# Kernel optimization log

Measured on AMD Instinct MI355X. Metric: run time of the kernel, lower is better.

The kernel has to match this reference:

```python
import jax, jax.numpy as jnp
import numpy as np

HIDDEN = 2048
NUM_HEADS = 16
NUM_KV_HEADS = 4
HEAD_DIM = HIDDEN // NUM_HEADS  # 128
WINDOW = 512
THETA = 10000.0
BATCH = 4
SEQ = 2048
NEG = -1e30


def _apply_rope(x, pos, theta):
    # x: [T, H, D] with interleaved even/odd rotation, matching the torch strided slicing
    half = x.shape[-1] // 2
    inv_freq = 1.0 / (theta ** (jnp.arange(half, dtype=jnp.float32) / half))
    ang = pos.astype(jnp.float32)[:, None] * inv_freq[None, :]          # [T, half]
    cos = jnp.cos(ang)[:, None, :]                                       # [T, 1, half]
    sin = jnp.sin(ang)[:, None, :]
    xe = x[..., 0::2].astype(jnp.float32)
    xo = x[..., 1::2].astype(jnp.float32)
    re = xe * cos - xo * sin
    ro = xe * sin + xo * cos
    out = jnp.stack([re, ro], axis=-1).reshape(x.shape)                  # re-interleave
    return out.astype(x.dtype)


def setup_inputs() -> dict:
    key = jax.random.key(0)
    ks = jax.random.split(key, 5)
    sc = 1.0 / np.sqrt(HIDDEN)
    hidden_states = jax.random.normal(ks[0], (BATCH * SEQ, HIDDEN), dtype=jnp.float32)
    q_w = jax.random.normal(ks[1], (HIDDEN, NUM_HEADS * HEAD_DIM), dtype=jnp.float32) * sc
    k_w = jax.random.normal(ks[2], (HIDDEN, NUM_KV_HEADS * HEAD_DIM), dtype=jnp.float32) * sc
    v_w = jax.random.normal(ks[3], (HIDDEN, NUM_KV_HEADS * HEAD_DIM), dtype=jnp.float32) * sc
    o_w = jax.random.normal(ks[4], (HIDDEN, HIDDEN), dtype=jnp.float32) * sc
    position_ids = jnp.tile(jnp.arange(SEQ, dtype=jnp.int32), BATCH)     # restart per sequence
    cu_seqlens = jnp.arange(BATCH + 1, dtype=jnp.int32) * SEQ
    return {
        "hidden_states": hidden_states, "q_w": q_w, "k_w": k_w, "v_w": v_w, "o_w": o_w,
        "position_ids": position_ids, "cu_seqlens": cu_seqlens, "max_seq_len": SEQ,
    }


def reference(hidden_states, q_w, k_w, v_w, o_w, position_ids, cu_seqlens, max_seq_len):
    T = hidden_states.shape[0]
    B = cu_seqlens.shape[0] - 1
    S = T // B  # equal-length packing
    groups = NUM_HEADS // NUM_KV_HEADS

    q = (hidden_states @ q_w).reshape(T, NUM_HEADS, HEAD_DIM)
    k = (hidden_states @ k_w).reshape(T, NUM_KV_HEADS, HEAD_DIM)
    v = (hidden_states @ v_w).reshape(T, NUM_KV_HEADS, HEAD_DIM)

    q = _apply_rope(q, position_ids, THETA)
    k = _apply_rope(k, position_ids, THETA)

    q = q.reshape(B, S, NUM_HEADS, HEAD_DIM)
    k = k.reshape(B, S, NUM_KV_HEADS, HEAD_DIM)
    v = v.reshape(B, S, NUM_KV_HEADS, HEAD_DIM)
    # GQA: expand kv heads to query heads
    k = jnp.repeat(k, groups, axis=2)   # [B, S, H, D]
    v = jnp.repeat(v, groups, axis=2)

    scale = 1.0 / np.sqrt(HEAD_DIM)
    scores = jnp.einsum('bqhd,bkhd->bhqk', q, k) * scale  # [B, H, S, S]

    pos = position_ids.reshape(B, S)
    pq = pos[:, None, :, None]
    pk = pos[:, None, None, :]
    # causal + sliding window (flash window_size=(WINDOW, 0) semantics): q-k in [0, WINDOW]
    allowed = (pk <= pq) & ((pq - pk) <= WINDOW)
    scores = jnp.where(allowed, scores, NEG)

    probs = jax.nn.softmax(scores, axis=-1)
    attn = jnp.einsum('bhqk,bkhd->bqhd', probs, v)        # [B, S, H, D]
    attn = attn.reshape(T, HIDDEN)
    return attn @ o_w
```

## Files before the change

### kernel.cpp

```cpp
#include <hip/hip_runtime.h>
#include <hip/hip_bf16.h>
#include <cstdint>
#include <cstddef>

typedef __bf16 bf16;
typedef __bf16 bf16x2 __attribute__((ext_vector_type(2)));
typedef __bf16 bf16x8 __attribute__((ext_vector_type(8)));
typedef float  f32x4  __attribute__((ext_vector_type(4)));

#define HIDDEN 2048
#define NHEADS 16
#define NKV    4
#define HD     128
#define WINDOW 512

__device__ __forceinline__ void gld16(const void* g, void* s) {
  __builtin_amdgcn_global_load_lds((const __attribute__((address_space(1))) void*)g,
                                   (__attribute__((address_space(3))) void*)s, 16, 0, 0);
}

__device__ __forceinline__ f32x4 mfma16(bf16x8 a, bf16x8 b, f32x4 c) {
  return __builtin_amdgcn_mfma_f32_16x16x32_bf16(a, b, c, 0, 0, 0);
}

__device__ __forceinline__ void barrier_raw() {
  asm volatile("" ::: "memory");
  __builtin_amdgcn_s_barrier();
  asm volatile("" ::: "memory");
}

__global__ __launch_bounds__(256) void cast_f32_bf16(const float* __restrict__ in,
                                                     bf16* __restrict__ out, int n4) {
  int i = blockIdx.x * 256 + threadIdx.x;
  if (i >= n4) return;
  f32x4 v = *(const f32x4*)(in + (size_t)i * 4);
  bf16x2 a, b;
  a[0] = (bf16)v[0]; a[1] = (bf16)v[1];
  b[0] = (bf16)v[2]; b[1] = (bf16)v[3];
  *(bf16x2*)(out + (size_t)i * 4)     = a;
  *(bf16x2*)(out + (size_t)i * 4 + 2) = b;
}

__global__ __launch_bounds__(256) void transpose_cast(const float* __restrict__ in,
                                                      bf16* __restrict__ out, int R, int C) {
  __shared__ float tile[32][33];
  int c0 = blockIdx.x * 32, r0 = blockIdx.y * 32;
  int tx = threadIdx.x, ty = threadIdx.y;
  #pragma unroll
  for (int i = 0; i < 4; ++i)
    tile[ty + i * 8][tx] = in[(size_t)(r0 + ty + i * 8) * C + c0 + tx];
  __syncthreads();
  #pragma unroll
  for (int i = 0; i < 4; ++i)
    out[(size_t)(c0 + ty + i * 8) * R + r0 + tx] = (bf16)tile[tx][ty + i * 8];
}

__device__ __forceinline__ void stage128x32(const bf16* __restrict__ A,
                                            const bf16* __restrict__ Bt,
                                            bf16* sA, bf16* sB,
                                            int m0, int n0, int K, int kt, int tid) {
  int wbase = tid & ~63;
  #pragma unroll
  for (int r = 0; r < 2; ++r) {
    int e = (r * 256 + tid) * 8;
    int row = e >> 5, col = e & 31;
    gld16(A  + (size_t)(m0 + row) * K + (size_t)kt * 32 + col,
          sA + (size_t)(r * 256 + wbase) * 8);
    gld16(Bt + (size_t)(n0 + row) * K + (size_t)kt * 32 + col,
          sB + (size_t)(r * 256 + wbase) * 8);
  }
}

__global__ __launch_bounds__(256) void gemm_bt(const bf16* __restrict__ A,
                                               const bf16* __restrict__ Bt,
                                               void* __restrict__ Cv,
                                               bf16* __restrict__ Vtout,
                                               int M, int N, int K, int outMode) {
  __shared__ bf16 sA[2][128 * 32];
  __shared__ bf16 sB[2][128 * 32];
  int nb = N >> 7;
  int perx = (int)gridDim.x >> 3;
  int bid0 = (int)blockIdx.x;
  int swzb = (bid0 & 7) * perx + (bid0 >> 3);
  int bm = swzb / nb, bn = swzb % nb;
  int m0 = bm << 7, n0 = bn << 7;
  int tid = threadIdx.x;
  int lane = tid & 63, w = tid >> 6;
  int li = lane & 15, g = lane >> 4, g8 = g * 8;
  int wm = w >> 1, wn = w & 1;
  f32x4 acc[4][4] = {};
  int NT = K >> 5;

  stage128x32(A, Bt, sA[0], sB[0], m0, n0, K, 0, tid);
  for (int kt = 0; kt < NT; ++kt) {
    int cur = kt & 1;
    asm volatile("s_waitcnt vmcnt(0)" ::: "memory");
    barrier_raw();
    if (kt + 1 < NT)
      stage128x32(A, Bt, sA[cur ^ 1], sB[cur ^ 1], m0, n0, K, kt + 1, tid);
    bf16x8 af[4], bv[4];
    #pragma unroll
    for (int mt = 0; mt < 4; ++mt)
      af[mt] = *(const bf16x8*)&sA[cur][(wm * 64 + mt * 16 + li) * 32 + g8];
    #pragma unroll
    for (int nt = 0; nt < 4; ++nt)
      bv[nt] = *(const bf16x8*)&sB[cur][(wn * 64 + nt * 16 + li) * 32 + g8];
    #pragma unroll
    for (int mt = 0; mt < 4; ++mt)
      #pragma unroll
      for (int nt = 0; nt < 4; ++nt)
        acc[mt][nt] = mfma16(af[mt], bv[nt], acc[mt][nt]);
  }
  #pragma unroll
  for (int mt = 0; mt < 4; ++mt)
    #pragma unroll
    for (int nt = 0; nt < 4; ++nt)
      #pragma unroll
      for (int j = 0; j < 4; ++j) {
        int row = m0 + wm * 64 + mt * 16 + g * 4 + j;
        int col = n0 + wn * 64 + nt * 16 + li;
        float v = acc[mt][nt][j];
        if (outMode == 0)      ((bf16*)Cv)[(size_t)row * N + col] = (bf16)v;
        else if (outMode == 1) ((bf16*)Cv)[(size_t)col * M + row] = (bf16)v;
        else if (outMode == 2) ((float*)Cv)[(size_t)row * N + col] = v;
        else {
          if (col < 512) ((bf16*)Cv)[(size_t)row * 512 + col] = (bf16)v;
          else           Vtout[(size_t)(col - 512) * M + row] = (bf16)v;
        }
      }
}

template<int RSP>
__device__ __forceinline__ void stage_quad(const bf16* __restrict__ G,
                                           bf16* __restrict__ sbuf,
                                           int grow0, int K, int k0, int half, int tid) {
  int w = tid >> 6, lane = tid & 63;
  int rl = lane >> 3;
  int col = ((lane & 7) ^ rl) * 8;
  #pragma unroll
  for (int r = 0; r < 2; ++r) {
    int lr0 = r * 64 + w * 8;
    int row0 = (lr0 & (RSP - 1)) + half * RSP + (lr0 / RSP) * 2 * RSP;
    gld16(G + (size_t)(grow0 + row0 + rl) * K + k0 + col,
          sbuf + row0 * 64);
  }
}

__global__ __launch_bounds__(512, 2) void gemm256(const bf16* __restrict__ A,
                                                  const bf16* __restrict__ Bt,
                                                  void* __restrict__ Cv,
                                                  int M, int N, int K, int outMode) {
  __shared__ bf16 sA[2][256 * 64];
  __shared__ bf16 sB[2][256 * 64];
  int nb = N >> 8;
  int cpx = (int)gridDim.x >> 3;
  int bid = (int)blockIdx.x;
  int swzb = (bid & 7) * cpx + (bid >> 3);
  int bm = swzb / nb, bn = swzb % nb;
  int m0 = bm << 8, n0 = bn << 8;
  int tid = threadIdx.x, lane = tid & 63, w = tid >> 6;
  int li = lane & 15, g = lane >> 4;
  int wm = w >> 2, wn = w & 3;
  int swz = (li & 7);

  f32x4 acc[8][4] = {};
  bf16x8 af[4][2];
  bf16x8 bv[2][2][2];

  int NT = K >> 6;

  stage_quad<64>(A,  sA[0], m0, K, 0, 0, tid);
  stage_quad<32>(Bt, sB[0], n0, K, 0, 0, tid);
  stage_quad<32>(Bt, sB[0], n0, K, 0, 1, tid);
  stage_quad<64>(A,  sA[0], m0, K, 0, 1, tid);

#define VMW(n) asm volatile("s_waitcnt vmcnt(" #n ")" ::: "memory")
#define SBAR() __builtin_amdgcn_sched_barrier(0)
#define LGKM(n) { asm volatile("s_waitcnt lgkmcnt(" #n ")" ::: "memory"); \
  __builtin_amdgcn_sched_barrier(0); }
#define LOAD_A256(mh) { _Pragma("unroll") for (int mf = 0; mf < 4; ++mf) \
  _Pragma("unroll") for (int ks = 0; ks < 2; ++ks) { \
    int row = wm * 128 + (mh) * 64 + mf * 16 + li; \
    af[mf][ks] = *(const bf16x8*)&sA[cur][row * 64 + ((ks * 4 + g) ^ swz) * 8]; } }
#define LOAD_B256(nh) { _Pragma("unroll") for (int nf = 0; nf < 2; ++nf) \
  _Pragma("unroll") for (int ks = 0; ks < 2; ++ks) { \
    int row = wn * 64 + (nh) * 32 + nf * 16 + li; \
    bv[nh][nf][ks] = *(const bf16x8*)&sB[cur][row * 64 + ((ks * 4 + g) ^ swz) * 8]; } }
#define MFMA_PH(mh, nh) { \
  __builtin_amdgcn_s_setprio(1); \
  _Pragma("unroll") for (int mf = 0; mf < 4; ++mf) \
  _Pragma("unroll") for (int nf = 0; nf < 2; ++nf) \
  _Pragma("unroll") for (int ks = 0; ks < 2; ++ks) \
    acc[(mh) * 4 + mf][(nh) * 2 + nf] = \
      mfma16(af[mf][ks], bv[nh][nf][ks], acc[(mh) * 4 + mf][(nh) * 2 + nf]); \
  __builtin_amdgcn_s_setprio(0); }

  int cur = 0;
  for (int t = 0; t < NT; ++t) {
    int nxt = cur ^ 1;
    bool pre = (t + 1 < NT);
    int k1 = (t + 1) << 6;
    VMW(0);
    barrier_raw();
    if (pre) stage_quad<64>(A, sA[nxt], m0, K, k1, 0, tid);
    LOAD_A256(0); LOAD_B256(0);
    SBAR();
    LOAD_B256(1);
    if (pre) stage_quad<32>(Bt, sB[nxt], n0, K, k1, 0, tid);
    LGKM(4);
    MFMA_PH(0, 0);
    if (pre) stage_quad<32>(Bt, sB[nxt], n0, K, k1, 1, tid);
    LGKM(0);
    MFMA_PH(0, 1);
    LOAD_A256(1);
    if (pre) stage_quad<64>(A, sA[nxt], m0, K, k1, 1, tid);
    LGKM(0);
    MFMA_PH(1, 1);
    MFMA_PH(1, 0);
    cur = nxt;
  }
#undef VMW
#undef SBAR
#undef LGKM
#undef LOAD_A256
#undef LOAD_B256
#undef MFMA_PH

  #pragma unroll
  for (int mi = 0; mi < 8; ++mi)
    #pragma unroll
    for (int ni = 0; ni < 4; ++ni)
      #pragma unroll
      for (int j = 0; j < 4; ++j) {
        int row = m0 + wm * 128 + mi * 16 + g * 4 + j;
        int col = n0 + wn * 64 + ni * 16 + li;
        float v = acc[mi][ni][j];
        if (outMode == 2) ((float*)Cv)[(size_t)row * N + col] = v;
        else              ((bf16*)Cv)[(size_t)row * N + col] = (bf16)v;
      }
}

__global__ __launch_bounds__(256) void rope_both(bf16* __restrict__ Qb,
                                                 bf16* __restrict__ Kb,
                                                 const int* __restrict__ pos, int T) {
  int idx = blockIdx.x * 256 + threadIdx.x;
  int total_q = T * NHEADS * 64;
  int total   = total_q + T * NKV * 64;
  if (idx >= total) return;
  bf16* X; int heads, local;
  if (idx < total_q) { X = Qb; heads = NHEADS; local = idx; }
  else               { X = Kb; heads = NKV;    local = idx - total_q; }
  int i = local & 63;
  int rest = local >> 6;
  int hh = rest % heads;
  int t = rest / heads;
  float inv = expf((float)i * (-9.210340371976184f / 64.0f));
  float ang = (float)pos[t] * inv;
  float s, c;
  sincosf(ang, &s, &c);
  bf16* p = X + ((size_t)t * heads + hh) * HD + 2 * i;
  bf16x2 xv = *(const bf16x2*)p;
  float xe = (float)xv[0], xo = (float)xv[1];
  bf16x2 r;
  r[0] = (bf16)(xe * c - xo * s);
  r[1] = (bf16)(xe * s + xo * c);
  *(bf16x2*)p = r;
}

__global__ __launch_bounds__(512) void attn_kernel(const bf16* __restrict__ Q,
                                                   const bf16* __restrict__ Kb,
                                                   const bf16* __restrict__ Vt,
                                                   const int* __restrict__ pos,
                                                   const int* __restrict__ cu,
                                                   bf16* __restrict__ O, int T, int B) {
  __shared__ bf16 sK[2][64 * 128];
  __shared__ bf16 sV[2][128 * 64];
  __shared__ bf16 sP[8][16 * 40];
  int bid = blockIdx.x;
  int nqb = T >> 6;
  int kvh = bid / nqb;
  int u   = bid % nqb;
  int qb  = (u & 7) * (nqb >> 3) + (u >> 3);
  int q0 = qb * 64;
  int tid = threadIdx.x, lane = tid & 63, w = tid >> 6;
  int hh = w & 3, rh = w >> 2;
  int h = kvh * 4 + hh;
  int li = lane & 15, g = lane >> 4, g8 = g * 8;
  int rb0 = q0 + rh * 32;

  int seq_start = 0, seq_end = T;
  for (int b = 0; b < B; ++b) {
    int a = cu[b], e = cu[b + 1];
    if (q0 >= a && q0 < e) { seq_start = a; seq_end = e; }
  }

  bf16x8 qf[2][4];
  #pragma unroll
  for (int grp = 0; grp < 2; ++grp)
    #pragma unroll
    for (int kd = 0; kd < 4; ++kd)
      qf[grp][kd] = *(const bf16x8*)(Q + (size_t)(rb0 + grp * 16 + li) * HIDDEN
                                     + h * HD + kd * 32 + g8);

  int pq[2][4], pmin[2], pmax[2];
  #pragma unroll
  for (int grp = 0; grp < 2; ++grp) {
    #pragma unroll
    for (int j = 0; j < 4; ++j) pq[grp][j] = pos[rb0 + grp * 16 + g * 4 + j];
    pmin[grp] = pos[rb0 + grp * 16];
    pmax[grp] = pos[rb0 + grp * 16 + 15];
  }

  float lsum[2][4] = {};
  f32x4 acc[2][8] = {};
  int kstart = q0 - WINDOW;
  if (kstart < seq_start) kstart = seq_start;
  int kend = q0 + 64;
  if (kend > seq_end) kend = seq_end;
  const float scale = 0.08838834764831845f;
  int nt = (kend - kstart) >> 6;

#define STAGE(kb_, buf_) { \
  _Pragma("unroll") for (int r = 0; r < 2; ++r) { \
    int n = r * 512 + tid; \
    int krow = n >> 4, kc = (n & 15) ^ (krow & 7); \
    gld16(Kb + (size_t)((kb_) + krow) * (NKV * HD) + kvh * HD + kc * 8, \
          &sK[buf_][(size_t)(r * 512 + (tid & ~63)) * 8]); \
    int vd = n >> 3, vc = (n & 7) ^ (vd & 7); \
    gld16(Vt + (size_t)(kvh * HD + vd) * T + (kb_) + vc * 8, \
          &sV[buf_][(size_t)(r * 512 + (tid & ~63)) * 8]); } }
#define VMW(n) asm volatile("s_waitcnt vmcnt(" #n ")" ::: "memory")

  STAGE(kstart, 0);
  for (int t = 0; t < nt; ++t) {
    int kb0 = kstart + t * 64;
    int cur = t & 1;
    VMW(0);
    barrier_raw();
    if (t + 1 < nt) STAGE(kb0 + 64, cur ^ 1);

    #pragma unroll
    for (int hhalf = 0; hhalf < 2; ++hhalf) {
      int kb = kb0 + hhalf * 32;
      int pkf = pos[kb], pkl = pos[kb + 31];
      int pk0 = pos[kb + li], pk1 = pos[kb + 16 + li];
      #pragma unroll
      for (int grp = 0; grp < 2; ++grp) {
        if (pkf > pmax[grp] || pkl < pmin[grp] - WINDOW) continue;
        f32x4 s0v = {0.f, 0.f, 0.f, 0.f}, s1v = {0.f, 0.f, 0.f, 0.f};
        #pragma unroll
        for (int kd = 0; kd < 4; ++kd) {
          int c0 = (kd * 4 + g) ^ (li & 7);
          bf16x8 b0 = *(const bf16x8*)&sK[cur][(hhalf * 32 + li) * 128 + c0 * 8];
          bf16x8 b1 = *(const bf16x8*)&sK[cur][(hhalf * 32 + 16 + li) * 128 + c0 * 8];
          s0v = mfma16(qf[grp][kd], b0, s0v);
          s1v = mfma16(qf[grp][kd], b1, s1v);
        }
        bool interior = (pkl <= pmin[grp]) && (pmax[grp] - pkf <= WINDOW);
        if (interior) {
          #pragma unroll
          for (int j = 0; j < 4; ++j) {
            float p0 = __expf(s0v[j] * scale);
            float p1 = __expf(s1v[j] * scale);
            lsum[grp][j] += p0 + p1;
            sP[w][(g * 4 + j) * 40 + li]      = (bf16)p0;
            sP[w][(g * 4 + j) * 40 + 16 + li] = (bf16)p1;
          }
        } else {
          #pragma unroll
          for (int j = 0; j < 4; ++j) {
            int d0 = pq[grp][j] - pk0, d1 = pq[grp][j] - pk1;
            float p0 = (d0 >= 0 && d0 <= WINDOW) ? __expf(s0v[j] * scale) : 0.f;
            float p1 = (d1 >= 0 && d1 <= WINDOW) ? __expf(s1v[j] * scale) : 0.f;
            lsum[grp][j] += p0 + p1;
            sP[w][(g * 4 + j) * 40 + li]      = (bf16)p0;
            sP[w][(g * 4 + j) * 40 + 16 + li] = (bf16)p1;
          }
        }
        bf16x8 pa = *(const bf16x8*)&sP[w][li * 40 + g8];
        #pragma unroll
        for (int dt = 0; dt < 8; ++dt) {
          int d = dt * 16 + li;
          int vc2 = (hhalf * 4 + g) ^ (d & 7);
          bf16x8 vf = *(const bf16x8*)&sV[cur][d * 64 + vc2 * 8];
          acc[grp][dt] = mfma16(pa, vf, acc[grp][dt]);
        }
      }
    }
  }
#undef STAGE
#undef VMW

  #pragma unroll
  for (int grp = 0; grp < 2; ++grp)
    #pragma unroll
    for (int j = 0; j < 4; ++j) {
      float rs = lsum[grp][j];
      rs += __shfl_xor(rs, 1);
      rs += __shfl_xor(rs, 2);
      rs += __shfl_xor(rs, 4);
      rs += __shfl_xor(rs, 8);
      float invl = 1.0f / rs;
      size_t base = (size_t)(rb0 + grp * 16 + g * 4 + j) * HIDDEN + h * HD;
      #pragma unroll
      for (int dt = 0; dt < 8; ++dt)
        O[base + dt * 16 + li] = (bf16)(acc[grp][dt][j] * invl);
    }
}

extern "C" void kernel_launch(void* const* d_in, const int* in_sizes, int n_in,
                              void* d_out, int out_size, void* d_ws, size_t ws_size,
                              hipStream_t stream) {
  const float* X  = (const float*)d_in[0];
  const float* qw = (const float*)d_in[1];
  const float* kw = (const float*)d_in[2];
  const float* vw = (const float*)d_in[3];
  const float* ow = (const float*)d_in[4];
  const int* pos = (const int*)d_in[5];
  const int* cu  = (const int*)d_in[6];
  int T = in_sizes[0] / HIDDEN;
  int B = in_sizes[6] - 1;
  float* out = (float*)d_out;

  bf16* ws = (bf16*)d_ws;
  size_t off = 0;
  bf16* Xb    = ws + off; off += (size_t)T * HIDDEN;
  bf16* Qb    = ws + off; off += (size_t)T * HIDDEN;
  bf16* Kb    = ws + off; off += (size_t)T * (NKV * HD);
  bf16* Vt    = ws + off; off += (size_t)T * (NKV * HD);
  bf16* qwT   = ws + off; off += (size_t)HIDDEN * HIDDEN;
  bf16* kvwT  = ws + off; off += (size_t)1024 * HIDDEN;
  bf16* owT   = ws + off; off += (size_t)HIDDEN * HIDDEN;

  cast_f32_bf16<<<(T * HIDDEN / 4 + 255) / 256, 256, 0, stream>>>(X, Xb, T * HIDDEN / 4);

  dim3 tb(32, 8);
  transpose_cast<<<dim3(HIDDEN / 32, HIDDEN / 32), tb, 0, stream>>>(qw, qwT, HIDDEN, HIDDEN);
  transpose_cast<<<dim3(512 / 32, HIDDEN / 32), tb, 0, stream>>>(kw, kvwT, HIDDEN, 512);
  transpose_cast<<<dim3(512 / 32, HIDDEN / 32), tb, 0, stream>>>(vw, kvwT + (size_t)512 * HIDDEN, HIDDEN, 512);
  transpose_cast<<<dim3(HIDDEN / 32, HIDDEN / 32), tb, 0, stream>>>(ow, owT, HIDDEN, HIDDEN);

  gemm256<<<(T / 256) * (HIDDEN / 256), 512, 0, stream>>>(Xb, qwT, Qb, T, HIDDEN, HIDDEN, 0);
  gemm_bt<<<(T / 128) * (1024 / 128), 256, 0, stream>>>(Xb, kvwT, Kb, Vt, T, 1024, HIDDEN, 3);

  rope_both<<<(T * (NHEADS + NKV) * 64 + 255) / 256, 256, 0, stream>>>(Qb, Kb, pos, T);

  attn_kernel<<<(T / 64) * NKV, 512, 0, stream>>>(Qb, Kb, Vt, pos, cu, Qb, T, B);

  gemm256<<<(T / 256) * (HIDDEN / 256), 512, 0, stream>>>(Qb, owT, out, T, HIDDEN, HIDDEN, 2);
}
```

Measured before the change: 320.5 us.

## Double GEMM K-tile to 64 with XOR-swizzled LDS layout

Each GEMM k-step now stages a 128x64 tile instead of 128x32, halving the number of barrier/wait iterations. An XOR swizzle of the 16-byte chunk index by row is applied on both the global-to-LDS store and the fragment reads, to avoid LDS bank conflicts that the wider 128-byte row stride would otherwise cause. This doubles LDS use to 64KB per block and raises register pressure from the extra fragments, which may lower occupancy.

```diff
diff --git a/kernel.cpp b/kernel.cpp
--- a/kernel.cpp
+++ b/kernel.cpp
@@ -55,19 +55,20 @@
     out[(size_t)(c0 + ty + i * 8) * R + r0 + tx] = (bf16)tile[tx][ty + i * 8];
 }
 
-__device__ __forceinline__ void stage128x32(const bf16* __restrict__ A,
+__device__ __forceinline__ void stage128x64(const bf16* __restrict__ A,
                                             const bf16* __restrict__ Bt,
                                             bf16* sA, bf16* sB,
                                             int m0, int n0, int K, int kt, int tid) {
-  int wbase = tid & ~63;
-  #pragma unroll
-  for (int r = 0; r < 2; ++r) {
-    int e = (r * 256 + tid) * 8;
-    int row = e >> 5, col = e & 31;
-    gld16(A  + (size_t)(m0 + row) * K + (size_t)kt * 32 + col,
-          sA + (size_t)(r * 256 + wbase) * 8);
-    gld16(Bt + (size_t)(n0 + row) * K + (size_t)kt * 32 + col,
-          sB + (size_t)(r * 256 + wbase) * 8);
+  int wb = (tid & ~63) * 8;
+  #pragma unroll
+  for (int r = 0; r < 4; ++r) {
+    int n = r * 256 + tid;
+    int row = n >> 3;
+    int c = (n & 7) ^ (row & 7);
+    gld16(A  + (size_t)(m0 + row) * K + (size_t)kt * 64 + c * 8,
+          sA + (size_t)(r * 256 * 8) + wb);
+    gld16(Bt + (size_t)(n0 + row) * K + (size_t)kt * 64 + c * 8,
+          sB + (size_t)(r * 256 * 8) + wb);
   }
 }
 
@@ -76,8 +77,8 @@
                                                void* __restrict__ Cv,
                                                bf16* __restrict__ Vtout,
                                                int M, int N, int K, int outMode) {
-  __shared__ bf16 sA[2][128 * 32];
-  __shared__ bf16 sB[2][128 * 32];
+  __shared__ bf16 sA[2][128 * 64];
+  __shared__ bf16 sB[2][128 * 64];
   int nb = N >> 7;
   int perx = (int)gridDim.x >> 3;
   int bid0 = (int)blockIdx.x;
@@ -86,30 +87,39 @@
   int m0 = bm << 7, n0 = bn << 7;
   int tid = threadIdx.x;
   int lane = tid & 63, w = tid >> 6;
-  int li = lane & 15, g = lane >> 4, g8 = g * 8;
+  int li = lane & 15, g = lane >> 4;
   int wm = w >> 1, wn = w & 1;
+  int swz = li & 7;
   f32x4 acc[4][4] = {};
-  int NT = K >> 5;
-
-  stage128x32(A, Bt, sA[0], sB[0], m0, n0, K, 0, tid);
+  int NT = K >> 6;
+
+  stage128x64(A, Bt, sA[0], sB[0], m0, n0, K, 0, tid);
   for (int kt = 0; kt < NT; ++kt) {
     int cur = kt & 1;
     asm volatile("s_waitcnt vmcnt(0)" ::: "memory");
     barrier_raw();
     if (kt + 1 < NT)
-      stage128x32(A, Bt, sA[cur ^ 1], sB[cur ^ 1], m0, n0, K, kt + 1, tid);
-    bf16x8 af[4], bv[4];
+      stage128x64(A, Bt, sA[cur ^ 1], sB[cur ^ 1], m0, n0, K, kt + 1, tid);
+    bf16x8 af[4][2], bv[4][2];
     #pragma unroll
     for (int mt = 0; mt < 4; ++mt)
-      af[mt] = *(const bf16x8*)&sA[cur][(wm * 64 + mt * 16 + li) * 32 + g8];
+      #pragma unroll
+      for (int ks = 0; ks < 2; ++ks)
+        af[mt][ks] = *(const bf16x8*)&sA[cur][(wm * 64 + mt * 16 + li) * 64
+                                              + ((ks * 4 + g) ^ swz) * 8];
     #pragma unroll
     for (int nt = 0; nt < 4; ++nt)
-      bv[nt] = *(const bf16x8*)&sB[cur][(wn * 64 + nt * 16 + li) * 32 + g8];
+      #pragma unroll
+      for (int ks = 0; ks < 2; ++ks)
+        bv[nt][ks] = *(const bf16x8*)&sB[cur][(wn * 64 + nt * 16 + li) * 64
+                                              + ((ks * 4 + g) ^ swz) * 8];
     #pragma unroll
     for (int mt = 0; mt < 4; ++mt)
       #pragma unroll
       for (int nt = 0; nt < 4; ++nt)
-        acc[mt][nt] = mfma16(af[mt], bv[nt], acc[mt][nt]);
+        #pragma unroll
+        for (int ks = 0; ks < 2; ++ks)
+          acc[mt][nt] = mfma16(af[mt][ks], bv[nt][ks], acc[mt][nt]);
   }
   #pragma unroll
   for (int mt = 0; mt < 4; ++mt)
```

New measurement: 308.5 us. 3.7% less time.
